# Kernel optimization log

Hardware: AMD Instinct MI355X
Metric: run time of the kernel (lower is better)

## Reference

```python
import jax, jax.numpy as jnp
import numpy as np

L, H, V, T, E = 12, 12, 50257, 1024, 768
DH = E // H
EPS = 1e-5


def _ln(x, g, b):
    mu = jnp.mean(x, axis=-1, keepdims=True)
    var = jnp.mean(jnp.square(x - mu), axis=-1, keepdims=True)
    return g * (x - mu) * jax.lax.rsqrt(var + EPS) + b


def _gelu(x):
    # tanh-approx gelu as in the source
    return 0.5 * x * (1.0 + jnp.tanh(jnp.sqrt(2.0 / jnp.pi) * (x + 0.044715 * jnp.power(x, 3))))


def setup_inputs() -> dict:
    key = jax.random.key(0)
    ks = jax.random.split(key, 12)
    s = 0.02
    return {
        "x": jax.random.randint(ks[0], (8, T), 0, V),
        "tok_emb": jax.random.normal(ks[1], (V, E), jnp.float32) * s,
        "pos_emb": jax.random.normal(ks[2], (T, E), jnp.float32) * s,
        "ln1_g": jnp.ones((L, E), jnp.float32),
        "ln1_b": jnp.zeros((L, E), jnp.float32),
        "Wqkv": jax.random.normal(ks[3], (L, E, 3 * E), jnp.float32) * s,
        "bqkv": jnp.zeros((L, 3 * E), jnp.float32),
        "Wo": jax.random.normal(ks[4], (L, E, E), jnp.float32) * s,
        "bo": jnp.zeros((L, E), jnp.float32),
        "ln2_g": jnp.ones((L, E), jnp.float32),
        "ln2_b": jnp.zeros((L, E), jnp.float32),
        "W1": jax.random.normal(ks[5], (L, E, 4 * E), jnp.float32) * s,
        "b1": jnp.zeros((L, 4 * E), jnp.float32),
        "W2": jax.random.normal(ks[6], (L, 4 * E, E), jnp.float32) * s,
        "b2": jnp.zeros((L, E), jnp.float32),
        "lnf_g": jnp.ones((E,), jnp.float32),
        "lnf_b": jnp.zeros((E,), jnp.float32),
    }


def _gpt2(x, tok_emb, pos_emb, ln1_g, ln1_b, Wqkv, bqkv, Wo, bo,
          ln2_g, ln2_b, W1, b1, W2, b2, lnf_g, lnf_b):
    B, S = x.shape
    h = tok_emb[x] + pos_emb[:S][None, :, :]  # [B,S,E]
    mask = (jnp.arange(S)[:, None] >= jnp.arange(S)[None, :]).astype(jnp.float32)  # [S,S]
    mask = mask[None, None]  # [1,1,S,S]
    scale = jax.lax.rsqrt(jnp.float32(DH))
    for l in range(L):
        a = _ln(h, ln1_g[l], ln1_b[l])
        qkv = jnp.einsum('bse,ef->bsf', a, Wqkv[l]) + bqkv[l]
        q, k, v = jnp.split(qkv, 3, axis=-1)
        q = q.reshape(B, S, H, DH).transpose(0, 2, 1, 3)
        k = k.reshape(B, S, H, DH).transpose(0, 2, 1, 3)
        v = v.reshape(B, S, H, DH).transpose(0, 2, 1, 3)
        w = jnp.einsum('bhqd,bhkd->bhqk', q, k) * scale
        w = w * mask - 1e10 * (1.0 - mask)
        w = jax.nn.softmax(w, axis=-1)
        ctx = jnp.einsum('bhqk,bhkd->bhqd', w, v)
        ctx = ctx.transpose(0, 2, 1, 3).reshape(B, S, E)
        h = h + jnp.einsum('bse,ef->bsf', ctx, Wo[l]) + bo[l]
        a2 = _ln(h, ln2_g[l], ln2_b[l])
        ff = _gelu(jnp.einsum('bse,ef->bsf', a2, W1[l]) + b1[l])
        h = h + jnp.einsum('bsf,fe->bse', ff, W2[l]) + b2[l]
    h = _ln(h, lnf_g, lnf_b)
    last = h[:, -1, :]  # [B,E]
    return jnp.matmul(last, tok_emb.T)  # [B,V]


def reference(x, tok_emb, pos_emb, ln1_g, ln1_b, Wqkv, bqkv, Wo, bo,
              ln2_g, ln2_b, W1, b1, W2, b2, lnf_g, lnf_b):
    return _gpt2(x, tok_emb, pos_emb, ln1_g, ln1_b, Wqkv, bqkv, Wo, bo,
                 ln2_g, ln2_b, W1, b1, W2, b2, lnf_g, lnf_b)
```

## Files before the change

kernel.cpp:

```cpp
#include <hip/hip_runtime.h>
#include <math.h>

#define LNUM 12
#define HNUM 12
#define EMB 768
#define TSEQ 1024
#define BBATCH 8
#define VOCAB 50257
#define NTOK (BBATCH*TSEQ)

typedef unsigned short u16;
typedef __bf16 bf16_8 __attribute__((ext_vector_type(8)));
typedef float f32x4 __attribute__((ext_vector_type(4)));

__device__ __forceinline__ u16 f2bf(float f){
  unsigned u = __float_as_uint(f);
  u += 0x7fffu + ((u >> 16) & 1u);
  return (u16)(u >> 16);
}
__device__ __forceinline__ float wred(float v){
  #pragma unroll
  for (int m = 32; m; m >>= 1) v += __shfl_xor(v, m, 64);
  return v;
}

#define GLOAD_LDS16(g, l) \
  __builtin_amdgcn_global_load_lds((const __attribute__((address_space(1))) void*)(g), \
                                   (__attribute__((address_space(3))) void*)(l), 16, 0, 0)

template<int N> struct WCst { static constexpr int val = N; };

__global__ __launch_bounds__(256) void tcvt_kernel(const float* __restrict__ src,
                                                   u16* __restrict__ dst, int K, int N){
  __shared__ float tile[32][33];
  size_t off = (size_t)blockIdx.z * K * N;
  const float* s = src + off;
  u16* d = dst + off;
  int n0 = blockIdx.x * 32, k0 = blockIdx.y * 32;
  int tx = threadIdx.x & 31, ty = threadIdx.x >> 5;
  #pragma unroll
  for (int i = 0; i < 4; i++)
    tile[ty + i*8][tx] = s[(size_t)(k0 + ty + i*8) * N + n0 + tx];
  __syncthreads();
  #pragma unroll
  for (int i = 0; i < 4; i++){
    int n = ty + i*8;
    d[(size_t)(n0 + n) * K + k0 + tx] = f2bf(tile[tx][n]);
  }
}

__global__ __launch_bounds__(256) void embed_kernel(const int* __restrict__ x,
    const float* __restrict__ tok, const float* __restrict__ pos, float* __restrict__ h){
  int row = blockIdx.x;
  int t = row & (TSEQ - 1);
  int id = x[row];
  const float* te = tok + (size_t)id * EMB;
  const float* pe = pos + (size_t)t * EMB;
  float* hr = h + (size_t)row * EMB;
  for (int i = threadIdx.x; i < EMB; i += 256) hr[i] = te[i] + pe[i];
}

template<int OBF, int LAST>
__global__ __launch_bounds__(256) void ln_kernel(const float* __restrict__ x,
    const float* __restrict__ g, const float* __restrict__ b, void* __restrict__ out){
  int orow, row;
  if (LAST){ orow = blockIdx.x; row = blockIdx.x * TSEQ + (TSEQ - 1); }
  else     { orow = row = blockIdx.x; }
  const float* xr = x + (size_t)row * EMB;
  int tid = threadIdx.x;
  int wave = tid >> 6, lane = tid & 63;
  float v[3];
  float s = 0.f;
  #pragma unroll
  for (int i = 0; i < 3; i++){ v[i] = xr[tid + i*256]; s += v[i]; }
  __shared__ float red[4];
  s = wred(s);
  if (lane == 0) red[wave] = s;
  __syncthreads();
  float mu = (red[0] + red[1] + red[2] + red[3]) * (1.f / EMB);
  float ss = 0.f;
  #pragma unroll
  for (int i = 0; i < 3; i++){ float d = v[i] - mu; ss += d * d; }
  __syncthreads();
  ss = wred(ss);
  if (lane == 0) red[wave] = ss;
  __syncthreads();
  float var = (red[0] + red[1] + red[2] + red[3]) * (1.f / EMB);
  float rs = rsqrtf(var + 1e-5f);
  #pragma unroll
  for (int i = 0; i < 3; i++){
    int e = tid + i*256;
    float o = g[e] * (v[i] - mu) * rs + b[e];
    if (OBF) ((u16*)out)[(size_t)orow * EMB + e] = f2bf(o);
    else     ((float*)out)[(size_t)orow * EMB + e] = o;
  }
}

template<int BM, int EPI>
__global__ __launch_bounds__(512, 2) void gemm_ring(const u16* __restrict__ A,
    const u16* __restrict__ Bt, const float* __restrict__ bias,
    const float* __restrict__ resid, void* __restrict__ outp, int K, int N){
  constexpr int LA = BM / 128;
  constexpr int LOADS = LA + 2;
  constexpr int SLOTE = (BM + 256) * 32;
  constexpr int M_REP = BM / 32;
  __shared__ __align__(16) u16 lds[4 * SLOTE];
  const int tid = threadIdx.x;
  const int wave = tid >> 6, lane = tid & 63;
  const int q15 = lane & 15, ko = lane >> 4;
  const int wm = wave >> 2, wn = wave & 3;
  const int bm = blockIdx.y, bn = blockIdx.x;
  const int NT = K >> 5;

  const u16* gA0 = A  + (size_t)(bm*BM  + (tid >> 2)) * K + (tid & 3) * 8;
  const u16* gB0 = Bt + (size_t)(bn*256 + (tid >> 2)) * K + (tid & 3) * 8;
  u16* ldsW = lds + (tid >> 6) * 512;

#define STAGE(tt) do { \
    int _t = (tt); \
    const u16* _sa = gA0 + (size_t)_t * 32; \
    const u16* _sb = gB0 + (size_t)_t * 32; \
    u16* _ls = ldsW + (_t & 3) * SLOTE; \
    _Pragma("unroll") \
    for (int _i = 0; _i < LA; _i++) \
      GLOAD_LDS16(_sa + (size_t)_i * 128 * K, _ls + _i * 4096); \
    _Pragma("unroll") \
    for (int _i = 0; _i < 2; _i++) \
      GLOAD_LDS16(_sb + (size_t)_i * 128 * K, _ls + BM*32 + _i * 4096); \
  } while (0)

  f32x4 acc[M_REP][4];
  #pragma unroll
  for (int i = 0; i < M_REP; i++)
    #pragma unroll
    for (int j = 0; j < 4; j++){ f32x4 z = {0.f,0.f,0.f,0.f}; acc[i][j] = z; }

  const int aoff = (wm*(BM/2) + q15) * 32 + ko * 8;
  const int boff = BM*32 + (wn*64 + q15) * 32 + ko * 8;

  auto tile = [&](int t, auto wc, bool dostage){
    if (dostage) STAGE(t + 3);
    const u16* sA = lds + (t & 3) * SLOTE;
    bf16_8 af[M_REP], bfr[4];
    #pragma unroll
    for (int mi = 0; mi < M_REP; mi++) af[mi] = *(const bf16_8*)(sA + aoff + mi * 512);
    #pragma unroll
    for (int ni = 0; ni < 4; ni++)    bfr[ni] = *(const bf16_8*)(sA + boff + ni * 512);
    __builtin_amdgcn_s_setprio(1);
    #pragma unroll
    for (int mi = 0; mi < M_REP; mi++)
      #pragma unroll
      for (int ni = 0; ni < 4; ni++)
        acc[mi][ni] = __builtin_amdgcn_mfma_f32_16x16x32_bf16(af[mi], bfr[ni], acc[mi][ni], 0, 0, 0);
    __builtin_amdgcn_s_setprio(0);
    asm volatile("s_waitcnt vmcnt(%0)" :: "n"(decltype(wc)::val) : "memory");
    __builtin_amdgcn_sched_barrier(0);
    __builtin_amdgcn_s_barrier();
    __builtin_amdgcn_sched_barrier(0);
  };

  STAGE(0); STAGE(1); STAGE(2);
  asm volatile("s_waitcnt vmcnt(%0)" :: "n"(2 * LOADS) : "memory");
  __builtin_amdgcn_sched_barrier(0);
  __builtin_amdgcn_s_barrier();
  __builtin_amdgcn_sched_barrier(0);

  for (int t = 0; t < NT - 3; ++t) tile(t, WCst<2 * LOADS>{}, true);
  tile(NT - 3, WCst<LOADS>{}, false);
  tile(NT - 2, WCst<0>{}, false);
  tile(NT - 1, WCst<0>{}, false);
#undef STAGE

  const int colb = bn*256 + wn*64;
  const int rowb = bm*BM + wm*(BM/2);
  #pragma unroll
  for (int ni = 0; ni < 4; ni++){
    int col = colb + ni*16 + q15;
    float bv = bias[col];
    #pragma unroll
    for (int mi = 0; mi < M_REP; mi++){
      #pragma unroll
      for (int j = 0; j < 4; j++){
        int row = rowb + mi*16 + ko*4 + j;
        float v = acc[mi][ni][j] + bv;
        if (EPI == 1) v += resid[(size_t)row * N + col];
        if (EPI == 2){
          float y = 0.7978845608028654f * (v + 0.044715f * v * v * v);
          float e = __expf(fminf(2.f * y, 80.f));
          v = v * e / (e + 1.f);
        }
        if (EPI == 3 && col < 768) v *= 0.125f;
        if (EPI == 2 || EPI == 3) ((u16*)outp)[(size_t)row * N + col] = f2bf(v);
        else                      ((float*)outp)[(size_t)row * N + col] = v;
      }
    }
  }
}

__global__ __launch_bounds__(256) void vtrans_kernel(const u16* __restrict__ qkvb,
                                                     u16* __restrict__ vt){
  int wave = threadIdx.x >> 6, lane = threadIdx.x & 63;
  int bh = blockIdx.y, b = bh / HNUM, h = bh - b * HNUM;
  int t0 = blockIdx.x * 16 + wave * 4;
  const u16* src = qkvb + (size_t)b * TSEQ * 2304 + 1536 + h * 64 + lane;
  unsigned long long w = 0;
  #pragma unroll
  for (int i = 0; i < 4; i++)
    w |= (unsigned long long)src[(size_t)(t0 + i) * 2304] << (16 * i);
  *(unsigned long long*)(vt + ((size_t)bh * 64 + lane) * TSEQ + t0) = w;
}

__global__ __launch_bounds__(256, 2) void attn_mfma(const u16* __restrict__ qkvb,
                                                    const u16* __restrict__ vt,
                                                    u16* __restrict__ ctx){
  __shared__ u16 plds[4][64][40];
  const int wave = threadIdx.x >> 6, lane = threadIdx.x & 63;
  const int g = lane >> 4, q15 = lane & 15;
  const int bh = blockIdx.y, b = bh / HNUM, h = bh - b * HNUM;
  const int q0 = ((int)gridDim.x - 1 - (int)blockIdx.x) * 256 + wave * 64;
  const u16* qk  = qkvb + (size_t)b * TSEQ * 2304 + h * 64;
  const u16* vtb = vt + (size_t)bh * 64 * TSEQ;

#define LOADKV(kb_, kd, vd) do { \
    _Pragma("unroll") \
    for (int _kf = 0; _kf < 2; _kf++) \
      _Pragma("unroll") \
      for (int _kc = 0; _kc < 2; _kc++) \
        kd[_kf][_kc] = *(const bf16_8*)(qk + (size_t)((kb_) + _kf*16 + q15) * 2304 + 768 + _kc*32 + g*8); \
    _Pragma("unroll") \
    for (int _dc = 0; _dc < 4; _dc++) \
      vd[_dc] = *(const bf16_8*)(vtb + (size_t)(_dc*16 + q15) * TSEQ + (kb_) + g*8); \
  } while (0)

  bf16_8 qfr[4][2];
  #pragma unroll
  for (int qf = 0; qf < 4; qf++)
    #pragma unroll
    for (int kc = 0; kc < 2; kc++)
      qfr[qf][kc] = *(const bf16_8*)(qk + (size_t)(q0 + qf*16 + q15) * 2304 + kc*32 + g*8);

  f32x4 oacc[4][4];
  #pragma unroll
  for (int i = 0; i < 4; i++)
    #pragma unroll
    for (int j = 0; j < 4; j++){ f32x4 z = {0.f,0.f,0.f,0.f}; oacc[i][j] = z; }
  float mx[4] = {-1e30f,-1e30f,-1e30f,-1e30f}, lsum[4] = {0.f,0.f,0.f,0.f};

  const int kbmax = q0 + 32;
  bf16_8 kcur[2][2], vcur[4];
  LOADKV(0, kcur, vcur);

  for (int kb = 0; kb <= kbmax; kb += 32){
    bf16_8 knxt[2][2], vnxt[4];
    if (kb < kbmax) LOADKV(kb + 32, knxt, vnxt);

    f32x4 s[2][4];
    #pragma unroll
    for (int kf = 0; kf < 2; kf++)
      #pragma unroll
      for (int qf = 0; qf < 4; qf++){
        f32x4 z = {0.f,0.f,0.f,0.f};
        z = __builtin_amdgcn_mfma_f32_16x16x32_bf16(kcur[kf][0], qfr[qf][0], z, 0, 0, 0);
        z = __builtin_amdgcn_mfma_f32_16x16x32_bf16(kcur[kf][1], qfr[qf][1], z, 0, 0, 0);
        s[kf][qf] = z;
      }

    if (kb + 31 > q0){
      #pragma unroll
      for (int kf = 0; kf < 2; kf++)
        #pragma unroll
        for (int qf = 0; qf < 4; qf++)
          #pragma unroll
          for (int j = 0; j < 4; j++)
            if (kb + kf*16 + g*4 + j > q0 + qf*16 + q15) s[kf][qf][j] = -1e30f;
    }

    #pragma unroll
    for (int qf = 0; qf < 4; qf++){
      float sm = -1e30f;
      #pragma unroll
      for (int kf = 0; kf < 2; kf++)
        #pragma unroll
        for (int j = 0; j < 4; j++) sm = fmaxf(sm, s[kf][qf][j]);
      sm = fmaxf(sm, __shfl_xor(sm, 16, 64));
      sm = fmaxf(sm, __shfl_xor(sm, 32, 64));
      float mn = fmaxf(mx[qf], sm);
      float c = __expf(mx[qf] - mn);
      mx[qf] = mn;
      float ps = 0.f;
      unsigned long long pw[2];
      #pragma unroll
      for (int kf = 0; kf < 2; kf++){
        unsigned long long w = 0;
        #pragma unroll
        for (int j = 0; j < 4; j++){
          float p = __expf(s[kf][qf][j] - mn);
          ps += p;
          w |= (unsigned long long)f2bf(p) << (16 * j);
        }
        pw[kf] = w;
      }
      ps += __shfl_xor(ps, 16, 64);
      ps += __shfl_xor(ps, 32, 64);
      lsum[qf] = lsum[qf] * c + ps;
      *(unsigned long long*)&plds[wave][qf*16 + q15][g*4]      = pw[0];
      *(unsigned long long*)&plds[wave][qf*16 + q15][16 + g*4] = pw[1];
      #pragma unroll
      for (int j = 0; j < 4; j++){
        float cr = __shfl(c, g*4 + j, 64);
        #pragma unroll
        for (int dc = 0; dc < 4; dc++) oacc[qf][dc][j] *= cr;
      }
    }

    asm volatile("s_waitcnt lgkmcnt(0)" ::: "memory");
    __builtin_amdgcn_sched_barrier(0);

    bf16_8 pa[4];
    #pragma unroll
    for (int qf = 0; qf < 4; qf++)
      pa[qf] = *(const bf16_8*)&plds[wave][qf*16 + q15][g*8];
    #pragma unroll
    for (int qf = 0; qf < 4; qf++)
      #pragma unroll
      for (int dc = 0; dc < 4; dc++)
        oacc[qf][dc] = __builtin_amdgcn_mfma_f32_16x16x32_bf16(pa[qf], vcur[dc], oacc[qf][dc], 0, 0, 0);

    if (kb < kbmax){
      #pragma unroll
      for (int kf = 0; kf < 2; kf++)
        #pragma unroll
        for (int kc = 0; kc < 2; kc++) kcur[kf][kc] = knxt[kf][kc];
      #pragma unroll
      for (int dc = 0; dc < 4; dc++) vcur[dc] = vnxt[dc];
    }
  }
#undef LOADKV

  u16* cb = ctx + ((size_t)(b * TSEQ + q0)) * EMB + h * 64;
  #pragma unroll
  for (int qf = 0; qf < 4; qf++){
    float inv = 1.f / lsum[qf];
    #pragma unroll
    for (int j = 0; j < 4; j++){
      float ir = __shfl(inv, g*4 + j, 64);
      int row = qf*16 + g*4 + j;
      #pragma unroll
      for (int dc = 0; dc < 4; dc++)
        cb[(size_t)row * EMB + dc*16 + q15] = f2bf(oacc[qf][dc][j] * ir);
    }
  }
}

__global__ __launch_bounds__(256) void logits_kernel(const float* __restrict__ last,
    const float* __restrict__ tok, float* __restrict__ out){
  __shared__ float ls[BBATCH * EMB];
  for (int i = threadIdx.x; i < BBATCH * EMB; i += 256) ls[i] = last[i];
  __syncthreads();
  int wave = threadIdx.x >> 6, lane = threadIdx.x & 63;
  int v = blockIdx.x * 4 + wave;
  if (v >= VOCAB) return;
  const float* tp = tok + (size_t)v * EMB;
  float acc[BBATCH];
  #pragma unroll
  for (int b = 0; b < BBATCH; b++) acc[b] = 0.f;
  #pragma unroll
  for (int i = 0; i < EMB/64; i++){
    float tv = tp[i*64 + lane];
    #pragma unroll
    for (int b = 0; b < BBATCH; b++) acc[b] += tv * ls[b*EMB + i*64 + lane];
  }
  #pragma unroll
  for (int b = 0; b < BBATCH; b++){
    float r = wred(acc[b]);
    if (lane == 0) out[(size_t)b * VOCAB + v] = r;
  }
}

extern "C" void kernel_launch(void* const* d_in, const int* in_sizes, int n_in,
                              void* d_out, int out_size, void* d_ws, size_t ws_size,
                              hipStream_t stream){
  const int*   x    = (const int*)  d_in[0];
  const float* tok  = (const float*)d_in[1];
  const float* pos  = (const float*)d_in[2];
  const float* ln1g = (const float*)d_in[3];
  const float* ln1b = (const float*)d_in[4];
  const float* Wqkv = (const float*)d_in[5];
  const float* bqkv = (const float*)d_in[6];
  const float* Wo   = (const float*)d_in[7];
  const float* bo   = (const float*)d_in[8];
  const float* ln2g = (const float*)d_in[9];
  const float* ln2b = (const float*)d_in[10];
  const float* W1   = (const float*)d_in[11];
  const float* b1   = (const float*)d_in[12];
  const float* W2   = (const float*)d_in[13];
  const float* b2   = (const float*)d_in[14];
  const float* lnfg = (const float*)d_in[15];
  const float* lnfb = (const float*)d_in[16];

  char* p = (char*)d_ws;
  u16* wqkvT = (u16*)p;  p += (size_t)LNUM*2304*768*2;
  u16* woT   = (u16*)p;  p += (size_t)LNUM*768*768*2;
  u16* w1T   = (u16*)p;  p += (size_t)LNUM*3072*768*2;
  u16* w2T   = (u16*)p;  p += (size_t)LNUM*768*3072*2;
  float* h   = (float*)p; p += (size_t)NTOK*EMB*4;
  u16* abuf  = (u16*)p;  p += (size_t)NTOK*EMB*2;
  void* tmp  = (void*)p; p += (size_t)NTOK*2304*4;
  u16* vt    = (u16*)p;  p += (size_t)BBATCH*HNUM*64*TSEQ*2;
  float* lastb = (float*)p; p += (size_t)BBATCH*EMB*4;
  if (ws_size < (size_t)(p - (char*)d_ws)) return;

  tcvt_kernel<<<dim3(2304/32, 768/32, LNUM), 256, 0, stream>>>(Wqkv, wqkvT, 768, 2304);
  tcvt_kernel<<<dim3(768/32,  768/32, LNUM), 256, 0, stream>>>(Wo,   woT,   768, 768);
  tcvt_kernel<<<dim3(3072/32, 768/32, LNUM), 256, 0, stream>>>(W1,   w1T,   768, 3072);
  tcvt_kernel<<<dim3(768/32, 3072/32, LNUM), 256, 0, stream>>>(W2,   w2T,   3072, 768);
  embed_kernel<<<NTOK, 256, 0, stream>>>(x, tok, pos, h);

  u16* qkvb = (u16*)tmp;
  u16* ff   = (u16*)tmp;
  for (int l = 0; l < LNUM; l++){
    ln_kernel<1,0><<<NTOK, 256, 0, stream>>>(h, ln1g + l*EMB, ln1b + l*EMB, abuf);
    gemm_ring<128,3><<<dim3(2304/256, NTOK/128), 512, 0, stream>>>(
        abuf, wqkvT + (size_t)l*2304*768, bqkv + (size_t)l*2304, nullptr, qkvb, 768, 2304);
    vtrans_kernel<<<dim3(TSEQ/16, BBATCH*HNUM), 256, 0, stream>>>(qkvb, vt);
    attn_mfma<<<dim3(TSEQ/256, BBATCH*HNUM), 256, 0, stream>>>(qkvb, vt, abuf);
    gemm_ring<128,1><<<dim3(768/256, NTOK/128), 512, 0, stream>>>(
        abuf, woT + (size_t)l*768*768, bo + (size_t)l*768, h, h, 768, 768);
    ln_kernel<1,0><<<NTOK, 256, 0, stream>>>(h, ln2g + l*EMB, ln2b + l*EMB, abuf);
    gemm_ring<256,2><<<dim3(3072/256, NTOK/256), 512, 0, stream>>>(
        abuf, w1T + (size_t)l*3072*768, b1 + (size_t)l*3072, nullptr, ff, 768, 3072);
    gemm_ring<128,1><<<dim3(768/256, NTOK/128), 512, 0, stream>>>(
        ff, w2T + (size_t)l*768*3072, b2 + (size_t)l*768, h, h, 3072, 768);
  }
  ln_kernel<0,1><<<BBATCH, 256, 0, stream>>>(h, lnfg, lnfb, lastb);
  logits_kernel<<<(VOCAB + 3)/4, 256, 0, stream>>>(lastb, tok, (float*)d_out);
}
```

Baseline: 3.934 ms.

## Restructure GEMM tiles to fixed BM=128 with templated BN and 3-slot ring

The GEMM kernel now fixes the M tile at 128 and templates the N tile (256 for the QKV and FFN1 GEMMs, 128 for the Wo and FFN2 GEMMs). LDS is stored in an MFMA-fragment-ready layout so each lane reads contiguous 16-byte chunks. The ring drops from 4 slots to 3 with prefetch distance 2, and launch bounds move to 4 blocks per CU. The aim is to cut LDS use and raise occupancy, and to double grid size for the narrow N=768 GEMMs. In exchange each tile reuses less data, and the shallower prefetch may expose more memory latency.

```diff
diff --git a/kernel.cpp b/kernel.cpp
--- a/kernel.cpp
+++ b/kernel.cpp
@@ -96,37 +96,35 @@
   }
 }
 
-template<int BM, int EPI>
-__global__ __launch_bounds__(512, 2) void gemm_ring(const u16* __restrict__ A,
+template<int BN, int EPI>
+__global__ __launch_bounds__(512, 4) void gemm_ring(const u16* __restrict__ A,
     const u16* __restrict__ Bt, const float* __restrict__ bias,
     const float* __restrict__ resid, void* __restrict__ outp, int K, int N){
-  constexpr int LA = BM / 128;
-  constexpr int LOADS = LA + 2;
-  constexpr int SLOTE = (BM + 256) * 32;
-  constexpr int M_REP = BM / 32;
-  __shared__ __align__(16) u16 lds[4 * SLOTE];
-  const int tid = threadIdx.x;
+  constexpr int NB    = BN / 128;
+  constexpr int LOADS = 1 + NB;
+  constexpr int NWN   = BN / 64;
+  constexpr int M_REP = NWN;
+  constexpr int AGRP  = 8;
+  constexpr int BGRP  = BN / 16;
+  constexpr int SLOTE = (AGRP + BGRP) * 512;
+  __shared__ __align__(16) u16 lds[3 * SLOTE];
+  const int tid  = threadIdx.x;
   const int wave = tid >> 6, lane = tid & 63;
-  const int q15 = lane & 15, ko = lane >> 4;
-  const int wm = wave >> 2, wn = wave & 3;
-  const int bm = blockIdx.y, bn = blockIdx.x;
-  const int NT = K >> 5;
-
-  const u16* gA0 = A  + (size_t)(bm*BM  + (tid >> 2)) * K + (tid & 3) * 8;
-  const u16* gB0 = Bt + (size_t)(bn*256 + (tid >> 2)) * K + (tid & 3) * 8;
-  u16* ldsW = lds + (tid >> 6) * 512;
-
-#define STAGE(tt) do { \
+  const int q15  = lane & 15, ko = lane >> 4;
+  const int wm   = wave / NWN, wn = wave % NWN;
+  const int bm   = blockIdx.y, bn = blockIdx.x;
+  const int NT   = K >> 5;
+
+  const u16* gA = A  + (size_t)(bm*128 + wave*16      + q15) * K + ko * 8;
+  const u16* gB = Bt + (size_t)(bn*BN  + wave*NB*16   + q15) * K + ko * 8;
+
+#define STAGE(tt, so) do { \
     int _t = (tt); \
-    const u16* _sa = gA0 + (size_t)_t * 32; \
-    const u16* _sb = gB0 + (size_t)_t * 32; \
-    u16* _ls = ldsW + (_t & 3) * SLOTE; \
+    GLOAD_LDS16(gA + (size_t)_t * 32, lds + (so) + wave * 512); \
     _Pragma("unroll") \
-    for (int _i = 0; _i < LA; _i++) \
-      GLOAD_LDS16(_sa + (size_t)_i * 128 * K, _ls + _i * 4096); \
-    _Pragma("unroll") \
-    for (int _i = 0; _i < 2; _i++) \
-      GLOAD_LDS16(_sb + (size_t)_i * 128 * K, _ls + BM*32 + _i * 4096); \
+    for (int _i = 0; _i < NB; _i++) \
+      GLOAD_LDS16(gB + (size_t)_i * 16 * K + (size_t)_t * 32, \
+                  lds + (so) + (AGRP + wave * NB + _i) * 512); \
   } while (0)
 
   f32x4 acc[M_REP][4];
@@ -135,17 +133,15 @@
     #pragma unroll
     for (int j = 0; j < 4; j++){ f32x4 z = {0.f,0.f,0.f,0.f}; acc[i][j] = z; }
 
-  const int aoff = (wm*(BM/2) + q15) * 32 + ko * 8;
-  const int boff = BM*32 + (wn*64 + q15) * 32 + ko * 8;
-
-  auto tile = [&](int t, auto wc, bool dostage){
-    if (dostage) STAGE(t + 3);
-    const u16* sA = lds + (t & 3) * SLOTE;
+  auto tile = [&](int t, int ro, int so, auto wc, bool dostage, bool dosync){
+    if (dostage) STAGE(t + 2, so);
     bf16_8 af[M_REP], bfr[4];
     #pragma unroll
-    for (int mi = 0; mi < M_REP; mi++) af[mi] = *(const bf16_8*)(sA + aoff + mi * 512);
-    #pragma unroll
-    for (int ni = 0; ni < 4; ni++)    bfr[ni] = *(const bf16_8*)(sA + boff + ni * 512);
+    for (int mi = 0; mi < M_REP; mi++)
+      af[mi] = *(const bf16_8*)(lds + ro + (wm*M_REP + mi) * 512 + lane * 8);
+    #pragma unroll
+    for (int ni = 0; ni < 4; ni++)
+      bfr[ni] = *(const bf16_8*)(lds + ro + (AGRP + wn*4 + ni) * 512 + lane * 8);
     __builtin_amdgcn_s_setprio(1);
     #pragma unroll
     for (int mi = 0; mi < M_REP; mi++)
@@ -153,26 +149,34 @@
       for (int ni = 0; ni < 4; ni++)
         acc[mi][ni] = __builtin_amdgcn_mfma_f32_16x16x32_bf16(af[mi], bfr[ni], acc[mi][ni], 0, 0, 0);
     __builtin_amdgcn_s_setprio(0);
-    asm volatile("s_waitcnt vmcnt(%0)" :: "n"(decltype(wc)::val) : "memory");
-    __builtin_amdgcn_sched_barrier(0);
-    __builtin_amdgcn_s_barrier();
-    __builtin_amdgcn_sched_barrier(0);
+    if (dosync){
+      asm volatile("s_waitcnt vmcnt(%0)" :: "n"(decltype(wc)::val) : "memory");
+      __builtin_amdgcn_sched_barrier(0);
+      __builtin_amdgcn_s_barrier();
+      __builtin_amdgcn_sched_barrier(0);
+    }
   };
 
-  STAGE(0); STAGE(1); STAGE(2);
-  asm volatile("s_waitcnt vmcnt(%0)" :: "n"(2 * LOADS) : "memory");
+  STAGE(0, 0);
+  STAGE(1, SLOTE);
+  asm volatile("s_waitcnt vmcnt(%0)" :: "n"(LOADS) : "memory");
   __builtin_amdgcn_sched_barrier(0);
   __builtin_amdgcn_s_barrier();
   __builtin_amdgcn_sched_barrier(0);
 
-  for (int t = 0; t < NT - 3; ++t) tile(t, WCst<2 * LOADS>{}, true);
-  tile(NT - 3, WCst<LOADS>{}, false);
-  tile(NT - 2, WCst<0>{}, false);
-  tile(NT - 1, WCst<0>{}, false);
+  int t = 0;
+  for (; t < NT - 3; t += 3){
+    tile(t,     0,         2*SLOTE, WCst<LOADS>{}, true,  true);
+    tile(t + 1, SLOTE,     0,       WCst<LOADS>{}, true,  true);
+    tile(t + 2, 2*SLOTE,   SLOTE,   WCst<LOADS>{}, true,  true);
+  }
+  tile(NT - 3, 0,       2*SLOTE, WCst<LOADS>{}, true,  true);
+  tile(NT - 2, SLOTE,   0,       WCst<0>{},     false, true);
+  tile(NT - 1, 2*SLOTE, 0,       WCst<0>{},     false, false);
 #undef STAGE
 
-  const int colb = bn*256 + wn*64;
-  const int rowb = bm*BM + wm*(BM/2);
+  const int colb = bn*BN  + wn * 64;
+  const int rowb = bm*128 + wm * (M_REP * 16);
   #pragma unroll
   for (int ni = 0; ni < 4; ni++){
     int col = colb + ni*16 + q15;
@@ -420,16 +424,16 @@
   u16* ff   = (u16*)tmp;
   for (int l = 0; l < LNUM; l++){
     ln_kernel<1,0><<<NTOK, 256, 0, stream>>>(h, ln1g + l*EMB, ln1b + l*EMB, abuf);
-    gemm_ring<128,3><<<dim3(2304/256, NTOK/128), 512, 0, stream>>>(
+    gemm_ring<256,3><<<dim3(2304/256, NTOK/128), 512, 0, stream>>>(
         abuf, wqkvT + (size_t)l*2304*768, bqkv + (size_t)l*2304, nullptr, qkvb, 768, 2304);
     vtrans_kernel<<<dim3(TSEQ/16, BBATCH*HNUM), 256, 0, stream>>>(qkvb, vt);
     attn_mfma<<<dim3(TSEQ/256, BBATCH*HNUM), 256, 0, stream>>>(qkvb, vt, abuf);
-    gemm_ring<128,1><<<dim3(768/256, NTOK/128), 512, 0, stream>>>(
+    gemm_ring<128,1><<<dim3(768/128, NTOK/128), 512, 0, stream>>>(
         abuf, woT + (size_t)l*768*768, bo + (size_t)l*768, h, h, 768, 768);
     ln_kernel<1,0><<<NTOK, 256, 0, stream>>>(h, ln2g + l*EMB, ln2b + l*EMB, abuf);
-    gemm_ring<256,2><<<dim3(3072/256, NTOK/256), 512, 0, stream>>>(
+    gemm_ring<256,2><<<dim3(3072/256, NTOK/128), 512, 0, stream>>>(
         abuf, w1T + (size_t)l*3072*768, b1 + (size_t)l*3072, nullptr, ff, 768, 3072);
-    gemm_ring<128,1><<<dim3(768/256, NTOK/128), 512, 0, stream>>>(
+    gemm_ring<128,1><<<dim3(768/128, NTOK/128), 512, 0, stream>>>(
         ff, w2T + (size_t)l*768*3072, b2 + (size_t)l*768, h, h, 3072, 768);
   }
   ln_kernel<0,1><<<BBATCH, 256, 0, stream>>>(h, lnfg, lnfb, lastb);
```

New measurement: 4.555 ms. 1.16x slower.
